# Kernel optimization log

Hardware: AMD Instinct MI355X
Metric: run time of the kernel (lower is better)

Reference implementation:

```python
import jax, jax.numpy as jnp
import numpy as np

N_EMBD = 1024
N_EXPERTS = 8
TOP_K = 2
D_FF = 4 * N_EMBD


def setup_inputs() -> dict:
    key = jax.random.key(0)
    ks = jax.random.split(key, 6)
    B, S = 4, 2048
    s = 1.0 / np.sqrt(N_EMBD)
    sf = 1.0 / np.sqrt(D_FF)
    x = jax.random.normal(ks[0], (B, S, N_EMBD), dtype=jnp.float32)
    router_w = jax.random.uniform(ks[1], (N_EMBD, N_EXPERTS), minval=-s, maxval=s, dtype=jnp.float32)
    wfc = jax.random.uniform(ks[2], (N_EXPERTS, N_EMBD, D_FF), minval=-s, maxval=s, dtype=jnp.float32)
    bfc = jax.random.uniform(ks[3], (N_EXPERTS, D_FF), minval=-s, maxval=s, dtype=jnp.float32)
    wproj = jax.random.uniform(ks[4], (N_EXPERTS, D_FF, N_EMBD), minval=-sf, maxval=sf, dtype=jnp.float32)
    bproj = jax.random.uniform(ks[5], (N_EXPERTS, N_EMBD), minval=-sf, maxval=sf, dtype=jnp.float32)
    return {"x": x, "router_w": router_w, "wfc": wfc, "bfc": bfc, "wproj": wproj, "bproj": bproj}


def reference(x, router_w, wfc, bfc, wproj, bproj):
    B, S, D = x.shape
    E = wfc.shape[0]
    xf = x.reshape(-1, D)  # [N, D] tokens
    logits = xf @ router_w  # [N, E]
    probs = jax.nn.softmax(logits.astype(jnp.float32), axis=-1)
    w, sel = jax.lax.top_k(probs, TOP_K)  # [N, K]
    w = w / jnp.sum(w, axis=-1, keepdims=True)  # norm_topk_prob
    w = w.astype(x.dtype)
    out = jnp.zeros_like(xf)
    for e in range(E):
        # per-token gate for expert e (0 if not routed here) -- same math as
        # gather -> MLP -> weighted scatter-add in the original
        gate = jnp.sum(jnp.where(sel == e, w, jnp.zeros_like(w)), axis=-1)  # [N]
        h = jax.nn.gelu(xf @ wfc[e] + bfc[e], approximate=False)  # [N, 4D]
        y = h @ wproj[e] + bproj[e]  # [N, D]
        out = out + gate[:, None] * y
    return out.reshape(B, S, D)
```

## Files before the change

kernel.cpp:

```cpp
#include <hip/hip_runtime.h>
#include <hip/hip_bf16.h>


#define N_TOK 8192
#define DMODEL 1024
#define NEXP 8
#define DFF 4096
#define CAP 8192

typedef __attribute__((ext_vector_type(8))) short short8;
typedef __attribute__((ext_vector_type(4))) float f32x4;

#define GLOAD_LDS16(g, l)                                              \
  __builtin_amdgcn_global_load_lds(                                    \
      (const __attribute__((address_space(1))) unsigned int*)(g),      \
      (__attribute__((address_space(3))) unsigned int*)(l), 16, 0, 0)

__device__ __forceinline__ unsigned short f2bf(float f) {
  unsigned u = __float_as_uint(f);
  return (unsigned short)((u + 0x7FFFu + ((u >> 16) & 1u)) >> 16);
}

__device__ __forceinline__ float gelu_f(float v) {
  return 0.5f * v * (1.0f + erff(v * 0.70710678118654752f));
}

__global__ void router_k(const float* __restrict__ x, const float* __restrict__ rw,
                         int* __restrict__ cnt, int* __restrict__ tok,
                         float* __restrict__ gate, unsigned short* __restrict__ xb) {
  int lane = threadIdx.x & 63;
  int t = blockIdx.x * 4 + (threadIdx.x >> 6);
  const float* xr = x + (size_t)t * DMODEL;
  unsigned short* xbr = xb + (size_t)t * DMODEL;
  float p[8];
#pragma unroll
  for (int e = 0; e < 8; ++e) p[e] = 0.0f;
#pragma unroll
  for (int j = 0; j < DMODEL / 64; ++j) {
    int i = lane + j * 64;
    float xv = xr[i];
    xbr[i] = f2bf(xv);
    const float4* r = (const float4*)(rw + (size_t)i * 8);
    float4 a = r[0], b = r[1];
    p[0] += xv * a.x; p[1] += xv * a.y; p[2] += xv * a.z; p[3] += xv * a.w;
    p[4] += xv * b.x; p[5] += xv * b.y; p[6] += xv * b.z; p[7] += xv * b.w;
  }
#pragma unroll
  for (int e = 0; e < 8; ++e) {
#pragma unroll
    for (int off = 32; off; off >>= 1) p[e] += __shfl_xor(p[e], off, 64);
  }
  if (lane == 0) {
    int e1 = 0;
#pragma unroll
    for (int e = 1; e < 8; ++e) if (p[e] > p[e1]) e1 = e;
    int e2 = (e1 == 0) ? 1 : 0;
#pragma unroll
    for (int e = 0; e < 8; ++e) if (e != e1 && p[e] > p[e2]) e2 = e;
    float w1 = 1.0f / (1.0f + expf(p[e2] - p[e1]));
    float w2 = 1.0f - w1;
    int s1 = atomicAdd(&cnt[e1], 1);
    tok[e1 * CAP + s1] = t; gate[e1 * CAP + s1] = w1;
    int s2 = atomicAdd(&cnt[e2], 1);
    tok[e2 * CAP + s2] = t; gate[e2 * CAP + s2] = w2;
  }
}

__global__ void prefix_k(const int* __restrict__ cnt, int* __restrict__ off) {
  if (threadIdx.x == 0 && blockIdx.x == 0) {
    int s = 0;
    for (int e = 0; e < NEXP; ++e) { off[e] = s; s += cnt[e]; }
  }
}

__global__ __launch_bounds__(256) void cvt_wt_k(const float* __restrict__ W,
                                                unsigned short* __restrict__ WT,
                                                int K, int N) {
  __shared__ float ls[64][68];
  int b = blockIdx.x;
  int nkt = K >> 6, nnt = N >> 6;
  int kt = b % nkt;
  int nt = (b / nkt) % nnt;
  int e = b / (nkt * nnt);
  const float* Wb = W + (size_t)e * K * N + (size_t)(kt * 64) * N + nt * 64;
  int t = threadIdx.x;
  int nn = (t & 15) * 4, kr = t >> 4;
#pragma unroll
  for (int i = 0; i < 4; ++i) {
    float4 v = *(const float4*)(Wb + (size_t)(kr + 16 * i) * N + nn);
    *(float4*)&ls[kr + 16 * i][nn] = v;
  }
  __syncthreads();
  int on = t >> 2, kc = (t & 3) * 16;
  unsigned short* dst = WT + (size_t)e * N * K + (size_t)(nt * 64 + on) * K + kt * 64 + kc;
  short8 r0, r1;
#pragma unroll
  for (int j = 0; j < 8; ++j) r0[j] = (short)f2bf(ls[kc + j][on]);
#pragma unroll
  for (int j = 0; j < 8; ++j) r1[j] = (short)f2bf(ls[kc + 8 + j][on]);
  *(short8*)dst = r0;
  *(short8*)(dst + 8) = r1;
}

#define STAGE(buf, kk)                                              \
  do {                                                              \
    GLOAD_LDS16(gA0 + (kk), &As[buf][(w * 32 + lr) * 32 + lc]);     \
    GLOAD_LDS16(gA1 + (kk), &As[buf][(w * 32 + 16 + lr) * 32 + lc]);\
    GLOAD_LDS16(gB0 + (kk), &Bs[buf][(w * 32 + lr) * 32 + lc]);     \
    GLOAD_LDS16(gB1 + (kk), &Bs[buf][(w * 32 + 16 + lr) * 32 + lc]);\
  } while (0)

#define COMPUTE(buf)                                                            \
  do {                                                                          \
    short8 af[4], bfv[4];                                                       \
    _Pragma("unroll") for (int i = 0; i < 4; ++i)                               \
        af[i] = *(const short8*)&As[buf][(wr * 64 + i * 16 + fr) * 32 + g * 8]; \
    _Pragma("unroll") for (int i = 0; i < 4; ++i)                               \
        bfv[i] = *(const short8*)&Bs[buf][(wc * 64 + i * 16 + fr) * 32 + g * 8];\
    _Pragma("unroll") for (int mi = 0; mi < 4; ++mi)                            \
        _Pragma("unroll") for (int ni = 0; ni < 4; ++ni)                        \
            acc[mi][ni] = __builtin_amdgcn_mfma_f32_16x16x32_bf16(              \
                af[mi], bfv[ni], acc[mi][ni], 0, 0, 0);                         \
  } while (0)

#define WAITV(n) asm volatile("s_waitcnt vmcnt(" #n ")" ::: "memory")
#define BAR() __builtin_amdgcn_s_barrier()

#define KLOOP(KTOT)                                                 \
  STAGE(0, 0);                                                      \
  STAGE(1, 32);                                                     \
  {                                                                 \
    int cur = 0;                                                    \
    _Pragma("unroll 1") for (int k0 = 0; k0 < (KTOT)-64; k0 += 32) {\
      WAITV(4);                                                     \
      BAR();                                                        \
      COMPUTE(cur);                                                 \
      BAR();                                                        \
      STAGE(cur, k0 + 64);                                          \
      cur ^= 1;                                                     \
    }                                                               \
    WAITV(4);                                                       \
    BAR();                                                          \
    COMPUTE(cur);                                                   \
    WAITV(0);                                                       \
    BAR();                                                          \
    COMPUTE(cur ^ 1);                                               \
  }

__global__ __launch_bounds__(256, 4) void gemm1a_k(
    const unsigned short* __restrict__ xb, const unsigned short* __restrict__ wT,
    const float* __restrict__ bfc, const int* __restrict__ cnt,
    const int* __restrict__ off, const int* __restrict__ tok,
    unsigned short* __restrict__ h) {
  int bid = (int)(blockIdx.x & 7) * ((int)gridDim.x >> 3) + (int)(blockIdx.x >> 3);
  int mt = bid & 63;
  int nt = (bid >> 6) & 31;
  int e = bid >> 11;
  int Me = cnt[e];
  if (mt * 128 >= Me) return;
  int base = off[e];
  int n0 = nt * 128;

  __shared__ __align__(16) unsigned short As[2][128 * 32];
  __shared__ __align__(16) unsigned short Bs[2][128 * 32];

  int tid = threadIdx.x;
  int lane = tid & 63, w = tid >> 6;
  int lr = lane >> 2;
  int lc = (lane & 3) * 8;

  int ar0i = mt * 128 + w * 32 + lr;
  int ar1i = ar0i + 16;
  int t0 = tok[e * CAP + ((ar0i < Me) ? ar0i : (Me - 1))];
  int t1 = tok[e * CAP + ((ar1i < Me) ? ar1i : (Me - 1))];
  const unsigned short* gA0 = xb + (size_t)t0 * DMODEL + lc;
  const unsigned short* gA1 = xb + (size_t)t1 * DMODEL + lc;
  const unsigned short* gB0 = wT + ((size_t)e * DFF + n0 + w * 32 + lr) * DMODEL + lc;
  const unsigned short* gB1 = gB0 + (size_t)16 * DMODEL;

  int wr = w >> 1, wc = w & 1;
  int g = lane >> 4, fr = lane & 15;

  f32x4 acc[4][4];
#pragma unroll
  for (int i = 0; i < 4; ++i)
#pragma unroll
    for (int j = 0; j < 4; ++j) acc[i][j] = (f32x4)0.0f;

  KLOOP(DMODEL);

#pragma unroll
  for (int mi = 0; mi < 4; ++mi) {
    int rl = wr * 64 + mi * 16 + g * 4;
#pragma unroll
    for (int i = 0; i < 4; ++i) {
      int r = mt * 128 + rl + i;
      if (r < Me) {
        unsigned short* hrow = h + (size_t)(base + r) * DFF;
#pragma unroll
        for (int ni = 0; ni < 4; ++ni) {
          int col = n0 + wc * 64 + ni * 16 + fr;
          float v = acc[mi][ni][i] + bfc[e * DFF + col];
          hrow[col] = f2bf(gelu_f(v));
        }
      }
    }
  }
}

__global__ __launch_bounds__(256, 4) void gemm2a_k(
    const unsigned short* __restrict__ h, const unsigned short* __restrict__ wT,
    const float* __restrict__ bproj, const int* __restrict__ cnt,
    const int* __restrict__ off, const int* __restrict__ tok,
    const float* __restrict__ gate, float* __restrict__ out) {
  int bid = (int)(blockIdx.x & 7) * ((int)gridDim.x >> 3) + (int)(blockIdx.x >> 3);
  int mt = bid & 63;
  int nt = (bid >> 6) & 7;
  int e = bid >> 9;
  int Me = cnt[e];
  if (mt * 128 >= Me) return;
  int base = off[e];
  int n0 = nt * 128;

  __shared__ __align__(16) unsigned short As[2][128 * 32];
  __shared__ __align__(16) unsigned short Bs[2][128 * 32];

  int tid = threadIdx.x;
  int lane = tid & 63, w = tid >> 6;
  int lr = lane >> 2;
  int lc = (lane & 3) * 8;

  const unsigned short* gA0 = h + (size_t)(base + mt * 128 + w * 32 + lr) * DFF + lc;
  const unsigned short* gA1 = gA0 + (size_t)16 * DFF;
  const unsigned short* gB0 = wT + ((size_t)e * DMODEL + n0 + w * 32 + lr) * DFF + lc;
  const unsigned short* gB1 = gB0 + (size_t)16 * DFF;

  int wr = w >> 1, wc = w & 1;
  int g = lane >> 4, fr = lane & 15;

  f32x4 acc[4][4];
#pragma unroll
  for (int i = 0; i < 4; ++i)
#pragma unroll
    for (int j = 0; j < 4; ++j) acc[i][j] = (f32x4)0.0f;

  KLOOP(DFF);

#pragma unroll
  for (int mi = 0; mi < 4; ++mi) {
    int rl = wr * 64 + mi * 16 + g * 4;
#pragma unroll
    for (int i = 0; i < 4; ++i) {
      int r = mt * 128 + rl + i;
      if (r < Me) {
        int tkn = tok[e * CAP + r];
        float gv = gate[e * CAP + r];
        float* orow = out + (size_t)tkn * DMODEL;
#pragma unroll
        for (int ni = 0; ni < 4; ++ni) {
          int col = n0 + wc * 64 + ni * 16 + fr;
          float v = acc[mi][ni][i] + bproj[e * DMODEL + col];
          atomicAdd(orow + col, gv * v);
        }
      }
    }
  }
}

extern "C" void kernel_launch(void* const* d_in, const int* in_sizes, int n_in,
                              void* d_out, int out_size, void* d_ws, size_t ws_size,
                              hipStream_t stream) {
  const float* x = (const float*)d_in[0];
  const float* rw = (const float*)d_in[1];
  const float* wfc = (const float*)d_in[2];
  const float* bfc = (const float*)d_in[3];
  const float* wproj = (const float*)d_in[4];
  const float* bproj = (const float*)d_in[5];
  float* out = (float*)d_out;

  char* ws = (char*)d_ws;
  int* cnt = (int*)ws;
  int* off_ = (int*)(ws + 64);
  int* tok = (int*)(ws + 4096);
  float* gate = (float*)(ws + 4096 + (size_t)NEXP * CAP * 4);
  size_t HOFF = 4096 + 2 * (size_t)NEXP * CAP * 4;
  unsigned short* h = (unsigned short*)(ws + HOFF);
  size_t HSZ = (size_t)(16384 + 128) * DFF * 2;
  size_t XOFF = HOFF + HSZ;
  size_t WOFF = XOFF + (size_t)N_TOK * DMODEL * 2;
  unsigned short* xb = (unsigned short*)(ws + XOFF);
  unsigned short* wT = (unsigned short*)(ws + WOFF);

  hipMemsetAsync(cnt, 0, 128, stream);
  hipMemsetAsync(out, 0, (size_t)out_size * 4, stream);
  router_k<<<N_TOK / 4, 256, 0, stream>>>(x, rw, cnt, tok, gate, xb);
  prefix_k<<<1, 64, 0, stream>>>(cnt, off_);
  cvt_wt_k<<<NEXP * (DMODEL / 64) * (DFF / 64), 256, 0, stream>>>(wfc, wT, DMODEL, DFF);
  gemm1a_k<<<NEXP * 32 * 64, 256, 0, stream>>>(xb, wT, bfc, cnt, off_, tok, h);
  cvt_wt_k<<<NEXP * (DFF / 64) * (DMODEL / 64), 256, 0, stream>>>(wproj, wT, DFF, DMODEL);
  gemm2a_k<<<NEXP * 8 * 64, 256, 0, stream>>>(h, wT, bproj, cnt, off_, tok, gate, out);
}
```

Before: 797.4 us.

## Add compact tile work list and triple-buffer LDS in expert GEMMs

Prefix kernel now builds a compact list of (expert, m-tile) work items so the GEMM grids launch only MAXW*N-tiles blocks instead of the full 64-m-tile worst case, removing the many early-exit blocks. The K loop moves from double to triple buffering of the A/B LDS tiles, deepening prefetch, and launch bounds drop to 3 blocks per CU to fit the larger shared memory. MAXW=136 bounds the total tiles; with top-2 routing over 8192 tokens there are 16384 assignments, and per-expert ceiling adds at most 8 tiles, so 136 covers it. The grid swizzle uses gridDim/8, which still divides evenly.

```diff
diff --git a/kernel.cpp b/kernel.cpp
--- a/kernel.cpp
+++ b/kernel.cpp
@@ -7,6 +7,7 @@
 #define NEXP 8
 #define DFF 4096
 #define CAP 8192
+#define MAXW 136
 
 typedef __attribute__((ext_vector_type(8))) short short8;
 typedef __attribute__((ext_vector_type(4))) float f32x4;
@@ -66,10 +67,17 @@
   }
 }
 
-__global__ void prefix_k(const int* __restrict__ cnt, int* __restrict__ off) {
+__global__ void prefix_k(const int* __restrict__ cnt, int* __restrict__ off,
+                         int* __restrict__ nwork, int* __restrict__ wl) {
   if (threadIdx.x == 0 && blockIdx.x == 0) {
-    int s = 0;
-    for (int e = 0; e < NEXP; ++e) { off[e] = s; s += cnt[e]; }
+    int s = 0, n = 0;
+    for (int e = 0; e < NEXP; ++e) {
+      off[e] = s;
+      int ntile = (cnt[e] + 127) >> 7;
+      for (int mt = 0; mt < ntile; ++mt) wl[n++] = (e << 16) | mt;
+      s += cnt[e];
+    }
+    nwork[0] = n;
   }
 }
 
@@ -129,40 +137,49 @@
 #define KLOOP(KTOT)                                                 \
   STAGE(0, 0);                                                      \
   STAGE(1, 32);                                                     \
+  STAGE(2, 64);                                                     \
   {                                                                 \
     int cur = 0;                                                    \
-    _Pragma("unroll 1") for (int k0 = 0; k0 < (KTOT)-64; k0 += 32) {\
-      WAITV(4);                                                     \
+    _Pragma("unroll 1") for (int k0 = 0; k0 + 96 < (KTOT); k0 += 32) {\
+      WAITV(8);                                                     \
       BAR();                                                        \
       COMPUTE(cur);                                                 \
       BAR();                                                        \
-      STAGE(cur, k0 + 64);                                          \
-      cur ^= 1;                                                     \
+      STAGE(cur, k0 + 96);                                          \
+      cur = (cur == 2) ? 0 : cur + 1;                               \
     }                                                               \
+    WAITV(8);                                                       \
+    BAR();                                                          \
+    COMPUTE(cur);                                                   \
+    cur = (cur == 2) ? 0 : cur + 1;                                 \
     WAITV(4);                                                       \
     BAR();                                                          \
     COMPUTE(cur);                                                   \
+    cur = (cur == 2) ? 0 : cur + 1;                                 \
     WAITV(0);                                                       \
     BAR();                                                          \
-    COMPUTE(cur ^ 1);                                               \
-  }
-
-__global__ __launch_bounds__(256, 4) void gemm1a_k(
+    COMPUTE(cur);                                                   \
+  }
+
+__global__ __launch_bounds__(256, 3) void gemm1a_k(
     const unsigned short* __restrict__ xb, const unsigned short* __restrict__ wT,
     const float* __restrict__ bfc, const int* __restrict__ cnt,
     const int* __restrict__ off, const int* __restrict__ tok,
+    const int* __restrict__ nwork, const int* __restrict__ wl,
     unsigned short* __restrict__ h) {
   int bid = (int)(blockIdx.x & 7) * ((int)gridDim.x >> 3) + (int)(blockIdx.x >> 3);
-  int mt = bid & 63;
-  int nt = (bid >> 6) & 31;
-  int e = bid >> 11;
+  int widx = bid % MAXW;
+  int nt = bid / MAXW;
+  if (widx >= nwork[0]) return;
+  int wle = wl[widx];
+  int e = wle >> 16;
+  int mt = wle & 0xffff;
   int Me = cnt[e];
-  if (mt * 128 >= Me) return;
   int base = off[e];
   int n0 = nt * 128;
 
-  __shared__ __align__(16) unsigned short As[2][128 * 32];
-  __shared__ __align__(16) unsigned short Bs[2][128 * 32];
+  __shared__ __align__(16) unsigned short As[3][128 * 32];
+  __shared__ __align__(16) unsigned short Bs[3][128 * 32];
 
   int tid = threadIdx.x;
   int lane = tid & 63, w = tid >> 6;
@@ -208,22 +225,25 @@
   }
 }
 
-__global__ __launch_bounds__(256, 4) void gemm2a_k(
+__global__ __launch_bounds__(256, 3) void gemm2a_k(
     const unsigned short* __restrict__ h, const unsigned short* __restrict__ wT,
     const float* __restrict__ bproj, const int* __restrict__ cnt,
     const int* __restrict__ off, const int* __restrict__ tok,
+    const int* __restrict__ nwork, const int* __restrict__ wl,
     const float* __restrict__ gate, float* __restrict__ out) {
   int bid = (int)(blockIdx.x & 7) * ((int)gridDim.x >> 3) + (int)(blockIdx.x >> 3);
-  int mt = bid & 63;
-  int nt = (bid >> 6) & 7;
-  int e = bid >> 9;
+  int widx = bid % MAXW;
+  int nt = bid / MAXW;
+  if (widx >= nwork[0]) return;
+  int wle = wl[widx];
+  int e = wle >> 16;
+  int mt = wle & 0xffff;
   int Me = cnt[e];
-  if (mt * 128 >= Me) return;
   int base = off[e];
   int n0 = nt * 128;
 
-  __shared__ __align__(16) unsigned short As[2][128 * 32];
-  __shared__ __align__(16) unsigned short Bs[2][128 * 32];
+  __shared__ __align__(16) unsigned short As[3][128 * 32];
+  __shared__ __align__(16) unsigned short Bs[3][128 * 32];
 
   int tid = threadIdx.x;
   int lane = tid & 63, w = tid >> 6;
@@ -281,6 +301,8 @@
   char* ws = (char*)d_ws;
   int* cnt = (int*)ws;
   int* off_ = (int*)(ws + 64);
+  int* nwork = (int*)(ws + 128);
+  int* wl = (int*)(ws + 256);
   int* tok = (int*)(ws + 4096);
   float* gate = (float*)(ws + 4096 + (size_t)NEXP * CAP * 4);
   size_t HOFF = 4096 + 2 * (size_t)NEXP * CAP * 4;
@@ -294,9 +316,9 @@
   hipMemsetAsync(cnt, 0, 128, stream);
   hipMemsetAsync(out, 0, (size_t)out_size * 4, stream);
   router_k<<<N_TOK / 4, 256, 0, stream>>>(x, rw, cnt, tok, gate, xb);
-  prefix_k<<<1, 64, 0, stream>>>(cnt, off_);
+  prefix_k<<<1, 64, 0, stream>>>(cnt, off_, nwork, wl);
   cvt_wt_k<<<NEXP * (DMODEL / 64) * (DFF / 64), 256, 0, stream>>>(wfc, wT, DMODEL, DFF);
-  gemm1a_k<<<NEXP * 32 * 64, 256, 0, stream>>>(xb, wT, bfc, cnt, off_, tok, h);
+  gemm1a_k<<<MAXW * 32, 256, 0, stream>>>(xb, wT, bfc, cnt, off_, tok, nwork, wl, h);
   cvt_wt_k<<<NEXP * (DFF / 64) * (DMODEL / 64), 256, 0, stream>>>(wproj, wT, DFF, DMODEL);
-  gemm2a_k<<<NEXP * 8 * 64, 256, 0, stream>>>(h, wT, bproj, cnt, off_, tok, gate, out);
-}
+  gemm2a_k<<<MAXW * 8, 256, 0, stream>>>(h, wT, bproj, cnt, off_, tok, nwork, wl, gate, out);
+}
```

Measured after the change: 827.0 us. 1.04x slower.
